# Performance work log

Measured on AMD Instinct MI355X. Metric: run time of the kernel, lower is better.

Reference implementation:

```python
import jax, jax.numpy as jnp
import numpy as np

B, M, D, OUT = 16384, 4096, 512, 128


def setup_inputs() -> dict:
    key = jax.random.key(0)
    ks = jax.random.split(key, 5)
    x = jax.random.normal(ks[0], (B, D), dtype=jnp.float32)
    support = jax.random.normal(ks[1], (M, D), dtype=jnp.float32)
    gamma = jnp.float32(1.0)
    head_w = jax.random.normal(ks[2], (OUT, M), dtype=jnp.float32) / np.sqrt(M)
    head_b = jax.random.normal(ks[3], (OUT,), dtype=jnp.float32) * 0.01
    scale = jnp.ones((1,), dtype=jnp.float32)
    shift = jnp.zeros((1,), dtype=jnp.float32)
    return {"x": x, "support": support, "gamma": gamma,
            "head_w": head_w, "head_b": head_b,
            "scale": scale, "shift": shift}


def reference(x, support, gamma, head_w, head_b, scale, shift):
    x2 = jnp.sum(x * x, axis=-1, keepdims=True)           # [B, 1]
    s2 = jnp.sum(support * support, axis=-1)              # [M]
    xs = jnp.einsum('bd,md->bm', x, support)              # [B, M]
    sqdist = jnp.maximum(x2 + s2[None, :] - 2.0 * xs, 0.0)
    k = jnp.exp(-gamma * sqdist)                          # RBF kernel [B, M]
    out = jnp.einsum('bm,om->bo', k, head_w) + head_b     # linear head [B, OUT]
    return scale * out + shift
```

## Files before the change

### kernel.cpp

```cpp
#include <hip/hip_runtime.h>

typedef unsigned int u32;
typedef unsigned short u16;
typedef unsigned char u8;
typedef __attribute__((ext_vector_type(8))) __bf16 bf16x8;
typedef __attribute__((ext_vector_type(4))) float f32x4;

#define NB 16384
#define NM 4096
#define ND 512
#define NOUT 128
#define L2E 1.44269504088896340736f


#define WAITVM(N) do { asm volatile("s_waitcnt vmcnt(" #N ")" ::: "memory"); \
                       __builtin_amdgcn_sched_barrier(0); } while (0)

__device__ __forceinline__ u16 f2bf(float f) {
  u32 u = __float_as_uint(f);
  u += 0x7FFFu + ((u >> 16) & 1u);
  return (u16)(u >> 16);
}

__device__ __forceinline__ u8 f2fp8(float f) {
  u32 u = __float_as_uint(f);
  u32 s = (u >> 24) & 0x80u;
  u32 au = u & 0x7FFFFFFFu;
  if (au < 0x3C800000u) return (u8)s;
  au += 0x000FFFFFu + ((au >> 20) & 1u);
  u32 e = (au >> 23) - 120u;
  u32 m = (au >> 20) & 7u;
  return (u8)(s | (e << 3) | m);
}

__device__ __forceinline__ void stage16(const void* g, void* l) {
  __builtin_amdgcn_global_load_lds((__attribute__((address_space(1))) void*)g,
                                   (__attribute__((address_space(3))) void*)l,
                                   16, 0, 0);
}

__device__ __forceinline__ uint4 pack8bf(float4 v0, float4 v1) {
  uint4 pk;
  pk.x = (u32)f2bf(v0.x) | ((u32)f2bf(v0.y) << 16);
  pk.y = (u32)f2bf(v0.z) | ((u32)f2bf(v0.w) << 16);
  pk.z = (u32)f2bf(v1.x) | ((u32)f2bf(v1.y) << 16);
  pk.w = (u32)f2bf(v1.z) | ((u32)f2bf(v1.w) << 16);
  return pk;
}

__device__ __forceinline__ uint2 pack8f8(float4 v0, float4 v1) {
  uint2 pk;
  pk.x = (u32)f2fp8(v0.x) | ((u32)f2fp8(v0.y) << 8) |
         ((u32)f2fp8(v0.z) << 16) | ((u32)f2fp8(v0.w) << 24);
  pk.y = (u32)f2fp8(v1.x) | ((u32)f2fp8(v1.y) << 8) |
         ((u32)f2fp8(v1.z) << 16) | ((u32)f2fp8(v1.w) << 24);
  return pk;
}

__global__ __launch_bounds__(256) void prep_all(const float* __restrict__ x,
                                                const float* __restrict__ s,
                                                const float* __restrict__ hw,
                                                const float* __restrict__ gamma_p,
                                                u8*  __restrict__ x_ws,
                                                u8*  __restrict__ s_ws,
                                                u16* __restrict__ hw_ws,
                                                float* __restrict__ x2g,
                                                float* __restrict__ s2g,
                                                float* __restrict__ out) {
  __shared__ uint2 t8[2048];
  __shared__ uint4 t16[2048];
  const int tid = threadIdx.x, bid = blockIdx.x;
  const int lane = tid & 63, w = tid >> 6;

  if (bid < 640) {
    const bool isx = bid < 512;
    const int blk = isx ? bid : (bid - 512);
    const float* src_m = isx ? x : s;
    u8*    dst_ws = isx ? x_ws : s_ws;
    float* sq_out = isx ? x2g : s2g;
    const float gl   = gamma_p[0] * L2E;
    const float cmul = isx ? 1.0f : (-2.0f * gl);
    const int big  = isx ? (blk >> 1) : (blk >> 2);
    const int roff = isx ? ((blk & 1) * 32) : ((blk & 3) * 32);
    const int rows = isx ? 64 : 128;

    #pragma unroll
    for (int p = 0; p < 8; ++p) {
      const int row = p * 4 + w;
      const float* src = src_m + (size_t)(blk * 32 + row) * ND + lane * 8;
      float4 v0 = *(const float4*)src;
      float4 v1 = *(const float4*)(src + 4);
      float ss = v0.x*v0.x + v0.y*v0.y + v0.z*v0.z + v0.w*v0.w
               + v1.x*v1.x + v1.y*v1.y + v1.z*v1.z + v1.w*v1.w;
      #pragma unroll
      for (int off = 32; off > 0; off >>= 1) ss += __shfl_down(ss, off);
      if (lane == 0) sq_out[blk * 32 + row] = gl * ss;
      v0.x *= cmul; v0.y *= cmul; v0.z *= cmul; v0.w *= cmul;
      v1.x *= cmul; v1.y *= cmul; v1.z *= cmul; v1.w *= cmul;
      t8[lane * 32 + ((row + lane) & 31)] = pack8f8(v0, v1);
    }
    __syncthreads();
    #pragma unroll
    for (int p = 0; p < 8; ++p) {
      const int kg = p * 8 + (tid >> 5);
      const int row = tid & 31;
      uint2 pk = t8[kg * 32 + ((row + kg) & 31)];
      *(uint2*)&dst_ws[(((size_t)(big * 64 + kg)) * rows + roff + row) * 8] = pk;
    }
  } else if (bid < 672) {
    const int blk = bid - 640;
    #pragma unroll
    for (int p = 0; p < 8; ++p) {
      const int o = p * 16 + (tid >> 4);
      const int kg = tid & 15;
      const float* src = hw + (size_t)o * NM + blk * 128 + kg * 8;
      float4 v0 = *(const float4*)src;
      float4 v1 = *(const float4*)(src + 4);
      t16[o * 16 + ((kg + o) & 15)] = pack8bf(v0, v1);
    }
    __syncthreads();
    #pragma unroll
    for (int it = 0; it < 8; ++it) {
      const int kg = it * 2 + (tid >> 7);
      const int o = tid & 127;
      uint4 pk = t16[o * 16 + ((kg + o) & 15)];
      *(uint4*)&hw_ws[(((size_t)(blk * 16 + kg)) * 128 + o) * 8] = pk;
    }
  } else {
    float4* o4 = (float4*)out;
    const float4 z = {0.f, 0.f, 0.f, 0.f};
    size_t base = (size_t)(bid - 672) * 8192 + tid;
    #pragma unroll 8
    for (int i = 0; i < 32; ++i) o4[base + (size_t)i * 256] = z;
  }
}

__global__ __launch_bounds__(256, 2)
void rbf_fused(const u8* __restrict__ x_ws, const u8* __restrict__ s_ws,
               const u16* __restrict__ hw_ws, const float* __restrict__ x2g,
               const float* __restrict__ s2g, const float* __restrict__ head_b,
               const float* __restrict__ scale_p, const float* __restrict__ shift_p,
               float* __restrict__ out)
{
  __shared__ __align__(16) char smem[65536];

  const int tid  = threadIdx.x;
  const int w    = tid >> 6;
  const int lane = tid & 63;
  const int quad = lane >> 4;
  const int l16  = lane & 15;
  const int wr   = w & 1;
  const int wc   = w >> 1;
  const int xcd  = blockIdx.x & 7;
  const int rb   = (blockIdx.x >> 3) * 2 + (xcd & 1);
  const int half = xcd >> 1;
  const int b0   = rb * 64;

  const float vscale = scale_p[0];
  const float vshift = shift_p[0];

  const u8* xsrc = x_ws + (size_t)rb * 32768;
  const u8* ssrc = s_ws + (size_t)(half * 8) * 65536;

  #pragma unroll
  for (int i = 0; i < 8; ++i)
    stage16(xsrc + i * 4096 + tid * 16, smem + i * 4096 + tid * 16);

  f32x4 x2v[2];
  #pragma unroll
  for (int r = 0; r < 2; ++r)
    x2v[r] = *(const f32x4*)&x2g[b0 + wr * 32 + r * 16 + quad * 4];

  const f32x4 zf = {0.f, 0.f, 0.f, 0.f};
  f32x4 acc_xs[2][4];
  f32x4 acc_out[2][4];
  #pragma unroll
  for (int r = 0; r < 2; ++r)
    #pragma unroll
    for (int c = 0; c < 4; ++c) { acc_xs[r][c] = zf; acc_out[r][c] = zf; }

  auto stage_sgrp = [&](int mt, int grp, int buf) {
    const u8* sp = ssrc + (size_t)mt * 65536 + grp * 8192;
    char* dp = smem + 32768 + buf * 8192;
    stage16(sp + tid * 16, dp + tid * 16);
    stage16(sp + 4096 + tid * 16, dp + 4096 + tid * 16);
  };

  auto compute_kc = [&](int kc, int kcL, int buf) {
    long long a[2], b[4];
    #pragma unroll
    for (int r = 0; r < 2; ++r)
      a[r] = *(const long long*)(smem + ((kc * 4 + quad) * 64 + wr * 32 + r * 16 + l16) * 8);
    #pragma unroll
    for (int c = 0; c < 4; ++c)
      b[c] = *(const long long*)(smem + 32768 + buf * 8192 +
                                 ((kcL * 4 + quad) * 128 + wc * 64 + c * 16 + l16) * 8);
    #pragma unroll
    for (int r = 0; r < 2; ++r)
      #pragma unroll
      for (int c = 0; c < 4; ++c)
        acc_xs[r][c] = __builtin_amdgcn_mfma_f32_16x16x32_fp8_fp8(a[r], b[c], acc_xs[r][c], 0, 0, 0);
  };

  auto g2_load = [&](int mtg2, int ks, bf16x8* b2) {
    const int kg = ks * 4 + quad;
    const size_t slab = (size_t)(mtg2 * 16 + kg);
    #pragma unroll
    for (int c = 0; c < 4; ++c)
      b2[c] = *(const bf16x8*)(hw_ws + (slab * 128 + wc * 64 + c * 16 + l16) * 8);
  };

  auto gemm2_mma = [&](int ks, const bf16x8* b2) {
    const int kg = ks * 4 + quad;
    bf16x8 a2[2];
    #pragma unroll
    for (int r = 0; r < 2; ++r)
      a2[r] = *(const bf16x8*)(smem + 49152 + (kg * 64 + wr * 32 + r * 16 + l16) * 16);
    #pragma unroll
    for (int r = 0; r < 2; ++r)
      #pragma unroll
      for (int c = 0; c < 4; ++c)
        acc_out[r][c] = __builtin_amdgcn_mfma_f32_16x16x32_bf16(a2[r], b2[c], acc_out[r][c], 0, 0, 0);
  };

  stage_sgrp(0, 0, 0);
  __syncthreads();

  #pragma unroll 1
  for (int mt = 0; mt < 8; ++mt) {
    const int mtg  = half * 8 + mt;
    const int mtg2 = mtg - (mt > 0);

    float s2v[4];
    #pragma unroll
    for (int c = 0; c < 4; ++c)
      s2v[c] = s2g[mtg * 128 + wc * 64 + c * 16 + l16];

    #pragma unroll
    for (int grp = 0; grp < 8; ++grp) {
      if (grp > 0) __builtin_amdgcn_s_barrier();

      bf16x8 b2[4];
      if ((grp & 1) == 0) g2_load(mtg2, grp >> 1, b2);

      if (grp < 7)      stage_sgrp(mt, grp + 1, (grp + 1) & 1);
      else if (mt < 7)  stage_sgrp(mt + 1, 0, 0);

      if (grp == 0)            WAITVM(10);
      else if (grp == 7)       { if (mt < 7) { WAITVM(2); } else { WAITVM(0); } }
      else if ((grp & 1) == 0) WAITVM(6);
      else                     WAITVM(2);
      __builtin_amdgcn_s_barrier();

      compute_kc(grp * 2,     0, grp & 1);
      compute_kc(grp * 2 + 1, 1, grp & 1);
      if (mt > 0 && (grp & 1) == 0) gemm2_mma(grp >> 1, b2);
    }

    {
      #pragma unroll
      for (int r = 0; r < 2; ++r)
        #pragma unroll
        for (int c = 0; c < 4; ++c) {
          const int cl = wc * 64 + c * 16 + l16;
          char* kbase = smem + 49152 + (cl >> 3) * 1024 + (cl & 7) * 2;
          #pragma unroll
          for (int i = 0; i < 4; ++i) {
            const int row = wr * 32 + r * 16 + quad * 4 + i;
            const float t = acc_xs[r][c][i] + x2v[r][i] + s2v[c];
            float kv = __builtin_amdgcn_exp2f(-t);
            kv = fminf(kv, 1.0f);
            *(u16*)(kbase + row * 16) = (u16)(__float_as_uint(kv) >> 16);
            acc_xs[r][c][i] = 0.0f;
          }
        }
    }
    asm volatile("s_waitcnt lgkmcnt(0)" ::: "memory");
    __builtin_amdgcn_sched_barrier(0);
    __builtin_amdgcn_s_barrier();
  }

  #pragma unroll
  for (int ks = 0; ks < 4; ++ks) {
    bf16x8 b2[4];
    g2_load(half * 8 + 7, ks, b2);
    gemm2_mma(ks, b2);
  }

  float addv[4];
  #pragma unroll
  for (int c = 0; c < 4; ++c) {
    const int col = wc * 64 + c * 16 + l16;
    addv[c] = (half == 0) ? (vscale * head_b[col] + vshift) : 0.0f;
  }
  #pragma unroll
  for (int r = 0; r < 2; ++r)
    #pragma unroll
    for (int c = 0; c < 4; ++c) {
      const int col = wc * 64 + c * 16 + l16;
      #pragma unroll
      for (int i = 0; i < 4; ++i) {
        const int row = b0 + wr * 32 + r * 16 + quad * 4 + i;
        atomicAdd(&out[(size_t)row * NOUT + col], vscale * acc_out[r][c][i] + addv[c]);
      }
    }
}

extern "C" void kernel_launch(void* const* d_in, const int* in_sizes, int n_in,
                              void* d_out, int out_size, void* d_ws, size_t ws_size,
                              hipStream_t stream) {
  const float* x       = (const float*)d_in[0];
  const float* support = (const float*)d_in[1];
  const float* gamma   = (const float*)d_in[2];
  const float* head_w  = (const float*)d_in[3];
  const float* head_b  = (const float*)d_in[4];
  const float* scale   = (const float*)d_in[5];
  const float* shift   = (const float*)d_in[6];
  float* out = (float*)d_out;

  char* w = (char*)d_ws;
  u8*    x_ws  = (u8*)(w);
  u8*    s_ws  = (u8*)(w + 8388608);
  u16*   hw_ws = (u16*)(w + 10485760);
  float* x2g   = (float*)(w + 11534336);
  float* s2g   = (float*)(w + 11599872);

  prep_all<<<736, 256, 0, stream>>>(x, support, head_w, gamma,
                                    x_ws, s_ws, hw_ws, x2g, s2g, out);
  rbf_fused<<<1024, 256, 0, stream>>>(x_ws, s_ws, hw_ws, x2g, s2g,
                                      head_b, scale, shift, out);
}
```

Measured before the change: 192.8 us.

## Deepen support staging to four LDS buffers and prefetch head weights earlier

Raises the support-tile pipeline from double to quad buffering (three groups in flight) using 80KB of dynamic LDS, and prefetches head_w fragments two groups ahead into ping-pong registers. LDS reads are hoisted before the barrier, and MFMA phases run at raised wave priority. The aim is to hide global-load latency behind the fp8 and bf16 MFMAs. The extra LDS (80KB per block) may reduce how many blocks fit per CU compared with the 2-block target in launch_bounds, and the added registers raise pressure.

```diff
diff --git a/kernel.cpp b/kernel.cpp
--- a/kernel.cpp
+++ b/kernel.cpp
@@ -13,8 +13,9 @@
 #define L2E 1.44269504088896340736f
 
 
-#define WAITVM(N) do { asm volatile("s_waitcnt vmcnt(" #N ")" ::: "memory"); \
+#define WAITLG(N) do { asm volatile("s_waitcnt vmcnt(" #N ") lgkmcnt(0)" ::: "memory"); \
                        __builtin_amdgcn_sched_barrier(0); } while (0)
+#define SB0() __builtin_amdgcn_sched_barrier(0)
 
 __device__ __forceinline__ u16 f2bf(float f) {
   u32 u = __float_as_uint(f);
@@ -142,7 +143,7 @@
                const float* __restrict__ scale_p, const float* __restrict__ shift_p,
                float* __restrict__ out)
 {
-  __shared__ __align__(16) char smem[65536];
+  extern __shared__ __align__(16) char smem[];
 
   const int tid  = threadIdx.x;
   const int w    = tid >> 6;
@@ -162,14 +163,30 @@
   const u8* xsrc = x_ws + (size_t)rb * 32768;
   const u8* ssrc = s_ws + (size_t)(half * 8) * 65536;
 
+  auto stage_grp = [&](int mt_s, int grp_s) {
+    const u8* sp = ssrc + (size_t)mt_s * 65536 + grp_s * 8192;
+    char* dp = smem + 32768 + (grp_s & 3) * 8192;
+    stage16(sp + tid * 16, dp + tid * 16);
+    stage16(sp + 4096 + tid * 16, dp + 4096 + tid * 16);
+  };
+
   #pragma unroll
   for (int i = 0; i < 8; ++i)
     stage16(xsrc + i * 4096 + tid * 16, smem + i * 4096 + tid * 16);
+  SB0();
 
   f32x4 x2v[2];
   #pragma unroll
   for (int r = 0; r < 2; ++r)
     x2v[r] = *(const f32x4*)&x2g[b0 + wr * 32 + r * 16 + quad * 4];
+
+  stage_grp(0, 0); SB0();
+  stage_grp(0, 1); SB0();
+  stage_grp(0, 2);
+  asm volatile("s_waitcnt vmcnt(4)" ::: "memory");
+  SB0();
+  __builtin_amdgcn_s_barrier();
+  SB0();
 
   const f32x4 zf = {0.f, 0.f, 0.f, 0.f};
   f32x4 acc_xs[2][4];
@@ -179,82 +196,88 @@
     #pragma unroll
     for (int c = 0; c < 4; ++c) { acc_xs[r][c] = zf; acc_out[r][c] = zf; }
 
-  auto stage_sgrp = [&](int mt, int grp, int buf) {
-    const u8* sp = ssrc + (size_t)mt * 65536 + grp * 8192;
-    char* dp = smem + 32768 + buf * 8192;
-    stage16(sp + tid * 16, dp + tid * 16);
-    stage16(sp + 4096 + tid * 16, dp + 4096 + tid * 16);
-  };
-
-  auto compute_kc = [&](int kc, int kcL, int buf) {
-    long long a[2], b[4];
-    #pragma unroll
-    for (int r = 0; r < 2; ++r)
-      a[r] = *(const long long*)(smem + ((kc * 4 + quad) * 64 + wr * 32 + r * 16 + l16) * 8);
-    #pragma unroll
-    for (int c = 0; c < 4; ++c)
-      b[c] = *(const long long*)(smem + 32768 + buf * 8192 +
-                                 ((kcL * 4 + quad) * 128 + wc * 64 + c * 16 + l16) * 8);
-    #pragma unroll
-    for (int r = 0; r < 2; ++r)
-      #pragma unroll
-      for (int c = 0; c < 4; ++c)
-        acc_xs[r][c] = __builtin_amdgcn_mfma_f32_16x16x32_fp8_fp8(a[r], b[c], acc_xs[r][c], 0, 0, 0);
-  };
-
-  auto g2_load = [&](int mtg2, int ks, bf16x8* b2) {
-    const int kg = ks * 4 + quad;
-    const size_t slab = (size_t)(mtg2 * 16 + kg);
-    #pragma unroll
-    for (int c = 0; c < 4; ++c)
-      b2[c] = *(const bf16x8*)(hw_ws + (slab * 128 + wc * 64 + c * 16 + l16) * 8);
-  };
-
-  auto gemm2_mma = [&](int ks, const bf16x8* b2) {
-    const int kg = ks * 4 + quad;
-    bf16x8 a2[2];
-    #pragma unroll
-    for (int r = 0; r < 2; ++r)
-      a2[r] = *(const bf16x8*)(smem + 49152 + (kg * 64 + wr * 32 + r * 16 + l16) * 16);
-    #pragma unroll
-    for (int r = 0; r < 2; ++r)
-      #pragma unroll
-      for (int c = 0; c < 4; ++c)
-        acc_out[r][c] = __builtin_amdgcn_mfma_f32_16x16x32_bf16(a2[r], b2[c], acc_out[r][c], 0, 0, 0);
-  };
-
-  stage_sgrp(0, 0, 0);
-  __syncthreads();
+  bf16x8 b2a[4], b2b[4];
 
   #pragma unroll 1
   for (int mt = 0; mt < 8; ++mt) {
-    const int mtg  = half * 8 + mt;
-    const int mtg2 = mtg - (mt > 0);
-
+    const int mtg = half * 8 + mt;
     float s2v[4];
-    #pragma unroll
-    for (int c = 0; c < 4; ++c)
-      s2v[c] = s2g[mtg * 128 + wc * 64 + c * 16 + l16];
 
     #pragma unroll
     for (int grp = 0; grp < 8; ++grp) {
-      if (grp > 0) __builtin_amdgcn_s_barrier();
-
-      bf16x8 b2[4];
-      if ((grp & 1) == 0) g2_load(mtg2, grp >> 1, b2);
-
-      if (grp < 7)      stage_sgrp(mt, grp + 1, (grp + 1) & 1);
-      else if (mt < 7)  stage_sgrp(mt + 1, 0, 0);
-
-      if (grp == 0)            WAITVM(10);
-      else if (grp == 7)       { if (mt < 7) { WAITVM(2); } else { WAITVM(0); } }
-      else if ((grp & 1) == 0) WAITVM(6);
-      else                     WAITVM(2);
+      if (grp == 0) {
+        #pragma unroll
+        for (int c = 0; c < 4; ++c)
+          s2v[c] = s2g[mtg * 128 + wc * 64 + c * 16 + l16];
+      }
+
+      long long a[2][2], b[2][4];
+      #pragma unroll
+      for (int k2 = 0; k2 < 2; ++k2) {
+        const int kc = grp * 2 + k2;
+        #pragma unroll
+        for (int r = 0; r < 2; ++r)
+          a[k2][r] = *(const long long*)(smem + ((kc * 4 + quad) * 64 + wr * 32 + r * 16 + l16) * 8);
+        #pragma unroll
+        for (int c = 0; c < 4; ++c)
+          b[k2][c] = *(const long long*)(smem + 32768 + (grp & 3) * 8192 +
+                                         ((k2 * 4 + quad) * 128 + wc * 64 + c * 16 + l16) * 8);
+      }
+
+      bf16x8 a2[2];
+      if (mt > 0 && (grp & 1) == 0) {
+        const int kg = (grp >> 1) * 4 + quad;
+        #pragma unroll
+        for (int r = 0; r < 2; ++r)
+          a2[r] = *(const bf16x8*)(smem + 65536 + (kg * 64 + wr * 32 + r * 16 + l16) * 16);
+      }
+
+      if ((grp & 1) == 0 && !(mt == 7 && grp == 6)) {
+        const int gc = (grp + 2) & 7;
+        const int mc = mt + (grp == 6);
+        int slab_mt = half * 8 + mc - 1; if (slab_mt < 0) slab_mt = 0;
+        const int kgc = (gc >> 1) * 4 + quad;
+        const size_t sb = (size_t)(slab_mt * 16 + kgc);
+        #pragma unroll
+        for (int c = 0; c < 4; ++c) {
+          bf16x8 v = *(const bf16x8*)(hw_ws + (sb * 128 + wc * 64 + c * 16 + l16) * 8);
+          if (((grp >> 1) & 1) == 0) b2a[c] = v; else b2b[c] = v;
+        }
+      }
+
+      SB0();
+
+      if (grp <= 4)      stage_grp(mt, grp + 3);
+      else if (mt < 7)   stage_grp(mt + 1, grp - 5);
+
+      if (grp == 0 || grp == 1)  WAITLG(12);
+      else if (grp <= 4)         WAITLG(8);
+      else if (grp == 5)         { if (mt < 7) WAITLG(8); else WAITLG(6); }
+      else                       { if (mt < 7) WAITLG(8); else WAITLG(0); }
+
       __builtin_amdgcn_s_barrier();
-
-      compute_kc(grp * 2,     0, grp & 1);
-      compute_kc(grp * 2 + 1, 1, grp & 1);
-      if (mt > 0 && (grp & 1) == 0) gemm2_mma(grp >> 1, b2);
+      SB0();
+
+      __builtin_amdgcn_s_setprio(1);
+      #pragma unroll
+      for (int k2 = 0; k2 < 2; ++k2)
+        #pragma unroll
+        for (int r = 0; r < 2; ++r)
+          #pragma unroll
+          for (int c = 0; c < 4; ++c)
+            acc_xs[r][c] = __builtin_amdgcn_mfma_f32_16x16x32_fp8_fp8(a[k2][r], b[k2][c],
+                                                                      acc_xs[r][c], 0, 0, 0);
+      if (mt > 0 && (grp & 1) == 0) {
+        #pragma unroll
+        for (int r = 0; r < 2; ++r)
+          #pragma unroll
+          for (int c = 0; c < 4; ++c) {
+            bf16x8 bb = ((((grp >> 1) + 1) & 1) == 0) ? b2a[c] : b2b[c];
+            acc_out[r][c] = __builtin_amdgcn_mfma_f32_16x16x32_bf16(a2[r], bb,
+                                                                    acc_out[r][c], 0, 0, 0);
+          }
+      }
+      __builtin_amdgcn_s_setprio(0);
     }
 
     {
@@ -263,7 +286,7 @@
         #pragma unroll
         for (int c = 0; c < 4; ++c) {
           const int cl = wc * 64 + c * 16 + l16;
-          char* kbase = smem + 49152 + (cl >> 3) * 1024 + (cl & 7) * 2;
+          char* kbase = smem + 65536 + (cl >> 3) * 1024 + (cl & 7) * 2;
           #pragma unroll
           for (int i = 0; i < 4; ++i) {
             const int row = wr * 32 + r * 16 + quad * 4 + i;
@@ -276,15 +299,27 @@
         }
     }
     asm volatile("s_waitcnt lgkmcnt(0)" ::: "memory");
-    __builtin_amdgcn_sched_barrier(0);
+    SB0();
     __builtin_amdgcn_s_barrier();
+    SB0();
   }
 
   #pragma unroll
   for (int ks = 0; ks < 4; ++ks) {
-    bf16x8 b2[4];
-    g2_load(half * 8 + 7, ks, b2);
-    gemm2_mma(ks, b2);
+    const int kg = ks * 4 + quad;
+    const size_t slab = (size_t)((half * 8 + 7) * 16 + kg);
+    bf16x8 b2[4], a2[2];
+    #pragma unroll
+    for (int c = 0; c < 4; ++c)
+      b2[c] = *(const bf16x8*)(hw_ws + (slab * 128 + wc * 64 + c * 16 + l16) * 8);
+    #pragma unroll
+    for (int r = 0; r < 2; ++r)
+      a2[r] = *(const bf16x8*)(smem + 65536 + (kg * 64 + wr * 32 + r * 16 + l16) * 16);
+    #pragma unroll
+    for (int r = 0; r < 2; ++r)
+      #pragma unroll
+      for (int c = 0; c < 4; ++c)
+        acc_out[r][c] = __builtin_amdgcn_mfma_f32_16x16x32_bf16(a2[r], b2[c], acc_out[r][c], 0, 0, 0);
   }
 
   float addv[4];
@@ -325,8 +360,15 @@
   float* x2g   = (float*)(w + 11534336);
   float* s2g   = (float*)(w + 11599872);
 
+  static bool lds_init = false;
+  if (!lds_init) {
+    hipFuncSetAttribute(reinterpret_cast<const void*>(rbf_fused),
+                        hipFuncAttributeMaxDynamicSharedMemorySize, 81920);
+    lds_init = true;
+  }
+
   prep_all<<<736, 256, 0, stream>>>(x, support, head_w, gamma,
                                     x_ws, s_ws, hw_ws, x2g, s2g, out);
-  rbf_fused<<<1024, 256, 0, stream>>>(x_ws, s_ws, hw_ws, x2g, s2g,
-                                      head_b, scale, shift, out);
-}
+  rbf_fused<<<1024, 256, 81920, stream>>>(x_ws, s_ws, hw_ws, x2g, s2g,
+                                          head_b, scale, shift, out);
+}
```

After: 176.2 us. 8.6% less time.
